# Optimization experiments

Hardware: AMD Instinct MI355X
Metric: run time of the kernel (lower is better)

The kernel has to match this reference:

```python
import jax, jax.numpy as jnp
import numpy as np

B, S, H, M, E = 64, 512, 1024, 26, 676  # batch, seq, hidden, max_nodes, max_edges (M*M)


def setup_inputs() -> dict:
    key = jax.random.key(0)
    ks = jax.random.split(key, 16)
    seq = jax.random.normal(ks[0], (B, S, H), jnp.float32)
    # ragged, strictly-increasing sentence-end offsets in [1, S-1], zero-padded tail
    rng = np.random.RandomState(0)
    off = np.zeros((B, M - 1), np.int64)
    for b in range(B):
        c = rng.randint(5, M)  # count of valid offsets per sample (ragged)
        off[b, :c] = np.sort(rng.choice(np.arange(1, S), size=c, replace=False))
    s = 1.0 / np.sqrt(H)
    s3 = 1.0 / np.sqrt(3 * H)
    return {
        'sequence_outputs': seq,
        'proof_offsets': jnp.asarray(off),
        'node_labels': jax.random.randint(ks[1], (B, M), 0, 2),
        'edge_labels': jax.random.randint(ks[2], (B, E), 0, 2),
        'W_naf': jax.random.normal(ks[3], (H, H), jnp.float32) * s,
        'b_naf': jnp.zeros((H,), jnp.float32),
        'W_cd': jax.random.normal(ks[4], (H, H), jnp.float32) * s,
        'b_cd': jnp.zeros((H,), jnp.float32),
        'W_co': jax.random.normal(ks[5], (H, 2), jnp.float32) * s,
        'b_co': jnp.zeros((2,), jnp.float32),
        'W_nd': jax.random.normal(ks[6], (H, H), jnp.float32) * s,
        'b_nd': jnp.zeros((H,), jnp.float32),
        'W_no': jax.random.normal(ks[7], (H, 2), jnp.float32) * s,
        'b_no': jnp.zeros((2,), jnp.float32),
        'W_ed': jax.random.normal(ks[8], (3 * H, H), jnp.float32) * s3,
        'b_ed': jnp.zeros((H,), jnp.float32),
        'W_eo': jax.random.normal(ks[9], (H, 2), jnp.float32) * s,
        'b_eo': jnp.zeros((2,), jnp.float32),
    }


def reference(sequence_outputs, proof_offsets, node_labels, edge_labels,
              W_naf, b_naf, W_cd, b_cd, W_co, b_co,
              W_nd, b_nd, W_no, b_no, W_ed, b_ed, W_eo, b_eo):
    Bx, Sx, Hx = sequence_outputs.shape
    Mx = node_labels.shape[1]
    Ex = edge_labels.shape[1]

    cls = sequence_outputs[:, 0, :]                       # [B,H]
    naf = cls @ W_naf + b_naf                             # NAF node embedding
    logits = jnp.tanh(cls @ W_cd + b_cd) @ W_co + b_co    # RobertaClassificationHead (eval: dropout=id)

    # segment-mean pooling via inclusive prefix sums: segment j = tokens (prev_j, off_j]
    P = jnp.cumsum(sequence_outputs, axis=1)              # [B,S,H]
    off = proof_offsets                                   # [B,M-1]
    prev = jnp.concatenate([jnp.zeros((Bx, 1), off.dtype), off[:, :-1]], axis=1)
    valid = off > 0                                       # [B,M-1]
    seg_sum = (jnp.take_along_axis(P, off[..., None], axis=1)
               - jnp.take_along_axis(P, prev[..., None], axis=1))  # [B,M-1,H]
    seg_len = jnp.maximum(off - prev, 1).astype(sequence_outputs.dtype)
    seg_mean = seg_sum / seg_len[..., None] * valid[..., None]

    count = valid.sum(axis=1)                             # nodes per sample (excl. NAF)
    # node embeddings: seg means at 0..count-1, NAF at index count, zeros after
    node_full = jnp.concatenate([seg_mean, jnp.zeros((Bx, 1, Hx), seg_mean.dtype)], axis=1)  # [B,M,H]
    idx = jnp.arange(Mx)
    node_full = node_full + (idx[None, :, None] == count[:, None, None]) * naf[:, None, :]

    # all-pairs edge features over n=count+1 nodes, row-major flat k=i*n+j, zero-padded to E
    n = count + 1                                         # [B]
    k = jnp.arange(Ex)                                    # [E]
    i = jnp.clip(k[None, :] // n[:, None], 0, Mx - 1)     # [B,E]
    j = jnp.clip(k[None, :] % n[:, None], 0, Mx - 1)
    valid_e = (k[None, :] < (n * n)[:, None])[..., None]
    ni = jnp.take_along_axis(node_full, i[..., None], axis=1)  # [B,E,H]
    nj = jnp.take_along_axis(node_full, j[..., None], axis=1)
    edge = jnp.concatenate([nj, ni, nj - ni], axis=-1) * valid_e  # [B,E,3H]

    node_logits = jnp.tanh(node_full @ W_nd + b_nd) @ W_no + b_no
    edge_logits = jnp.tanh(edge @ W_ed + b_ed) @ W_eo + b_eo
    return (logits, node_logits, edge_logits)
```

## Files before the change

kernel.cpp:

```cpp
#include <hip/hip_runtime.h>
#include <hip/hip_bf16.h>

#define B_ 64
#define S_ 512
#define H_ 1024
#define M_ 26
#define E_ 676

typedef short bf16x8 __attribute__((ext_vector_type(8)));
typedef float f32x4 __attribute__((ext_vector_type(4)));

__device__ __forceinline__ void gload16(const void* g, void* l) {
    __builtin_amdgcn_global_load_lds((const __attribute__((address_space(1))) unsigned int*)g,
                                     (__attribute__((address_space(3))) unsigned int*)l,
                                     16, 0, 0);
}

__device__ __forceinline__ float tanh_fast(float x) {
    float e = __expf(2.0f * x);
    return 1.0f - 2.0f * __builtin_amdgcn_rcpf(e + 1.0f);
}

__global__ __launch_bounds__(256) void k_stage1(
    const float* __restrict__ seq, const int* __restrict__ off,
    const float* __restrict__ Wnaf, const float* __restrict__ Wcd,
    const float* __restrict__ Wnd, const float* __restrict__ Wed,
    const float* __restrict__ bed, const float* __restrict__ Weo,
    const float* __restrict__ beo,
    __hip_bfloat16* __restrict__ Wt, int* __restrict__ count,
    float* __restrict__ econ, float* __restrict__ naf, float* __restrict__ cdh,
    float* __restrict__ node_sum) {
    __shared__ float smem[2048];
    int bid = blockIdx.x;
    int tid = threadIdx.x;

    if (bid < 2048) {
        int chunk = bid & 31, b = bid >> 5;
        int t0 = chunk * 16;
        const float4* sq = (const float4*)(seq + (size_t)b * S_ * H_);
        float4 buf[16];
#pragma unroll
        for (int i = 0; i < 16; ++i)
            buf[i] = sq[(size_t)(t0 + i) * (H_ / 4) + tid];

        int* offs = (int*)smem;
        int* cs = (int*)smem + 28;
        if (tid < M_ - 1) offs[tid] = off[b * (M_ - 1) + tid];
        __syncthreads();
        if (tid == 0) {
            int c = 0;
            while (c < M_ - 1 && offs[c] > 0) c++;
            cs[0] = c; cs[1] = (c > 0) ? offs[c - 1] : 0;
        }
        __syncthreads();
        int c = cs[0], offmax = cs[1];
        int ts = max(t0, 1), te = min(t0 + 15, offmax);
        int m = 0;
        while (m < c && offs[m] < ts) m++;
        float4 acc = make_float4(0, 0, 0, 0);
#pragma unroll
        for (int i = 0; i < 16; ++i) {
            int t = t0 + i;
            if (t < ts || t > te) continue;
            if (offs[m] < t) {
                float* dst = node_sum + ((size_t)(b * M_ + m)) * H_ + tid * 4;
                atomicAdd(dst + 0, acc.x); atomicAdd(dst + 1, acc.y);
                atomicAdd(dst + 2, acc.z); atomicAdd(dst + 3, acc.w);
                acc = make_float4(0, 0, 0, 0);
                while (offs[m] < t) m++;
            }
            acc.x += buf[i].x; acc.y += buf[i].y;
            acc.z += buf[i].z; acc.w += buf[i].w;
        }
        float* dst = node_sum + ((size_t)(b * M_ + m)) * H_ + tid * 4;
        atomicAdd(dst + 0, acc.x); atomicAdd(dst + 1, acc.y);
        atomicAdd(dst + 2, acc.z); atomicAdd(dst + 3, acc.w);
    } else if (bid < 2304) {
        float (*As)[64] = (float(*)[64])smem;
        float (*Bs)[64] = (float(*)[64])(smem + 1024);
        int e = bid - 2048;
        int bx = e & 31;
        int kbase = (e >> 5) * 128;
        const float* W;
        float* dst;
        int cbase;
        if (bx < 16) { W = Wnaf; dst = naf; cbase = bx * 64; }
        else         { W = Wcd;  dst = cdh; cbase = (bx - 16) * 64; }
        int tx = tid % 16, ty = tid / 16;
        float c[4][4] = {};
        int la_row = tid / 4;
        int la_k4  = (tid % 4) * 4;
        int lb_k   = tid / 16;
        int lb_c4  = (tid % 16) * 4;
        for (int k0 = 0; k0 < 128; k0 += 16) {
            float4 a = *(const float4*)(seq + (size_t)la_row * S_ * H_ + kbase + k0 + la_k4);
            *(float4*)(&Bs[lb_k][lb_c4]) =
                *(const float4*)(W + (size_t)(kbase + k0 + lb_k) * H_ + cbase + lb_c4);
            As[la_k4 + 0][la_row] = a.x;
            As[la_k4 + 1][la_row] = a.y;
            As[la_k4 + 2][la_row] = a.z;
            As[la_k4 + 3][la_row] = a.w;
            __syncthreads();
#pragma unroll
            for (int kk = 0; kk < 16; ++kk) {
                float4 av = *(const float4*)(&As[kk][ty * 4]);
                float4 bv = *(const float4*)(&Bs[kk][tx * 4]);
                c[0][0] += av.x * bv.x; c[0][1] += av.x * bv.y; c[0][2] += av.x * bv.z; c[0][3] += av.x * bv.w;
                c[1][0] += av.y * bv.x; c[1][1] += av.y * bv.y; c[1][2] += av.y * bv.z; c[1][3] += av.y * bv.w;
                c[2][0] += av.z * bv.x; c[2][1] += av.z * bv.y; c[2][2] += av.z * bv.z; c[2][3] += av.z * bv.w;
                c[3][0] += av.w * bv.x; c[3][1] += av.w * bv.y; c[3][2] += av.w * bv.z; c[3][3] += av.w * bv.w;
            }
            __syncthreads();
        }
#pragma unroll
        for (int i = 0; i < 4; ++i)
#pragma unroll
            for (int j = 0; j < 4; ++j)
                atomicAdd(dst + (size_t)(ty * 4 + i) * H_ + cbase + tx * 4 + j, c[i][j]);
    } else if (bid < 5376) {
        float (*T)[33] = (float(*)[33])smem;
        int idx = bid - 2304;
        int s = idx >> 10, rem = idx & 1023;
        int bx = rem & 31, by = rem >> 5;
        int c = tid & 31, r0 = tid >> 5;
        const int HH = H_ * H_;
#pragma unroll
        for (int i = 0; i < 4; ++i) {
            int r = r0 + 8 * i;
            size_t k = by * 32 + r, n = bx * 32 + c;
            float v;
            if (s == 0)      v = Wnd[k * H_ + n];
            else if (s == 1) v = Wed[k * H_ + n] + Wed[2 * HH + k * H_ + n];
            else             v = Wed[HH + k * H_ + n] - Wed[2 * HH + k * H_ + n];
            T[r][c] = v;
        }
        __syncthreads();
#pragma unroll
        for (int i = 0; i < 4; ++i) {
            int rr = r0 + 8 * i;
            Wt[(size_t)(s * H_ + bx * 32 + rr) * H_ + by * 32 + c] = __float2bfloat16(T[c][rr]);
        }
    } else if (bid == 5376) {
        if (tid < 64) {
            int b = tid;
            int c = 0;
            for (int m = 0; m < M_ - 1; ++m) c += (off[b * (M_ - 1) + m] > 0) ? 1 : 0;
            count[b] = c;
        }
    } else {
        float* s0 = smem; float* s1 = smem + 256;
        float a0 = 0.f, a1 = 0.f;
        for (int h = tid; h < H_; h += 256) {
            float t = tanh_fast(bed[h]);
            a0 += t * Weo[h * 2 + 0];
            a1 += t * Weo[h * 2 + 1];
        }
        s0[tid] = a0; s1[tid] = a1; __syncthreads();
        for (int o = 128; o > 0; o >>= 1) {
            if (tid < o) { s0[tid] += s0[tid + o]; s1[tid] += s1[tid + o]; }
            __syncthreads();
        }
        if (tid == 0) { econ[0] = s0[0] + beo[0]; econ[1] = s1[0] + beo[1]; }
    }
}

__global__ __launch_bounds__(256) void k_stage2(
    const float* __restrict__ sums, const int* __restrict__ off,
    const int* __restrict__ count, const float* __restrict__ naf,
    const float* __restrict__ bnaf, __hip_bfloat16* __restrict__ nodeB,
    const float* __restrict__ cdh, const float* __restrict__ bcd,
    const float* __restrict__ Wco, const float* __restrict__ bco,
    float* __restrict__ out) {
    __shared__ float smem[512];
    int bid = blockIdx.x;
    int tid = threadIdx.x;
    if (bid < 1664) {
        int b = bid / 26, m = bid - b * 26;
        int cnt = count[b];
        float4 v = make_float4(0, 0, 0, 0);
        const float4* row = (const float4*)(sums + ((size_t)(b * M_ + m)) * H_);
        if (m < M_ - 1) {
            int o = off[b * (M_ - 1) + m];
            if (o > 0) {
                int prev = (m > 0) ? off[b * (M_ - 1) + m - 1] : 0;
                float inv = 1.0f / (float)max(o - prev, 1);
                float4 s = row[tid];
                v = make_float4(s.x * inv, s.y * inv, s.z * inv, s.w * inv);
            }
        }
        if (m == cnt) {
            float4 a = ((const float4*)(naf + (size_t)b * H_))[tid];
            float4 bb = ((const float4*)bnaf)[tid];
            v.x += a.x + bb.x; v.y += a.y + bb.y; v.z += a.z + bb.z; v.w += a.w + bb.w;
        }
        __hip_bfloat16 __attribute__((aligned(8))) h[4] = {
            __float2bfloat16(v.x), __float2bfloat16(v.y),
            __float2bfloat16(v.z), __float2bfloat16(v.w)};
        *(ushort4*)(nodeB + ((size_t)(b * M_ + m)) * H_ + tid * 4) = *(const ushort4*)h;
    } else {
        int b = bid - 1664;
        float* s0 = smem; float* s1 = smem + 256;
        float a0 = 0.f, a1 = 0.f;
        for (int h = tid; h < H_; h += 256) {
            float t = tanh_fast(cdh[(size_t)b * H_ + h] + bcd[h]);
            a0 += t * Wco[h * 2 + 0];
            a1 += t * Wco[h * 2 + 1];
        }
        s0[tid] = a0; s1[tid] = a1; __syncthreads();
        for (int o = 128; o > 0; o >>= 1) {
            if (tid < o) { s0[tid] += s0[tid + o]; s1[tid] += s1[tid + o]; }
            __syncthreads();
        }
        if (tid == 0) { out[b * 2 + 0] = s0[0] + bco[0]; out[b * 2 + 1] = s1[0] + bco[1]; }
    }
}

#define GM 1664
#define GN 3072
#define GK 1024
__global__ __launch_bounds__(256) void k_mfma(const __hip_bfloat16* __restrict__ A,
                                              const __hip_bfloat16* __restrict__ Bt,
                                              float* __restrict__ C) {
    __shared__ __hip_bfloat16 As[128 * 32];
    __shared__ __hip_bfloat16 Bs[128 * 32];
    int tid = threadIdx.x;
    int wid = tid >> 6, ln = tid & 63;
    int row0 = blockIdx.y * 128, col0 = blockIdx.x * 128;
    const __hip_bfloat16* ga = A + (size_t)(row0 + wid * 16 + (ln >> 2)) * GK + (ln & 3) * 8;
    const __hip_bfloat16* gb = Bt + (size_t)(col0 + wid * 16 + (ln >> 2)) * GK + (ln & 3) * 8;
    __hip_bfloat16* lA = As + wid * 512;
    __hip_bfloat16* lB = Bs + wid * 512;
    int mrow = (wid >> 1) * 64, ncol = (wid & 1) * 64;
    int l15 = ln & 15, l4 = ln >> 4;
    f32x4 acc[4][4] = {};
    const __hip_bfloat16* pa = As + (size_t)(mrow + l15) * 32 + l4 * 8;
    const __hip_bfloat16* pb = Bs + (size_t)(ncol + l15) * 32 + l4 * 8;
    for (int k0 = 0; k0 < GK; k0 += 32) {
        gload16(ga, lA);
        gload16(ga + 64 * GK, lA + 2048);
        gload16(gb, lB);
        gload16(gb + 64 * GK, lB + 2048);
        ga += 32; gb += 32;
        __syncthreads();
        bf16x8 af[4], bf[4];
#pragma unroll
        for (int mi = 0; mi < 4; ++mi) af[mi] = *(const bf16x8*)(pa + mi * 16 * 32);
#pragma unroll
        for (int ni = 0; ni < 4; ++ni) bf[ni] = *(const bf16x8*)(pb + ni * 16 * 32);
#pragma unroll
        for (int mi = 0; mi < 4; ++mi)
#pragma unroll
            for (int ni = 0; ni < 4; ++ni)
                acc[mi][ni] = __builtin_amdgcn_mfma_f32_16x16x32_bf16(af[mi], bf[ni],
                                                                      acc[mi][ni], 0, 0, 0);
        __syncthreads();
    }
#pragma unroll
    for (int mi = 0; mi < 4; ++mi)
#pragma unroll
        for (int ni = 0; ni < 4; ++ni) {
            f32x4 v = acc[mi][ni];
            size_t r = row0 + mrow + mi * 16 + l4 * 4;
            size_t cc = col0 + ncol + ni * 16 + l15;
            C[(r + 0) * GN + cc] = v[0];
            C[(r + 1) * GN + cc] = v[1];
            C[(r + 2) * GN + cc] = v[2];
            C[(r + 3) * GN + cc] = v[3];
        }
}

__global__ __launch_bounds__(256) void k_stage4(
    const float* __restrict__ Cm, const int* __restrict__ count,
    const float* __restrict__ bnd, const float* __restrict__ Wno,
    const float* __restrict__ bno, const float* __restrict__ bed,
    const float* __restrict__ Weo, const float* __restrict__ beo,
    const float* __restrict__ econ, float* __restrict__ out_n,
    float* __restrict__ out_e) {
    int bid = blockIdx.x;
    int wid = threadIdx.x >> 6, lane = threadIdx.x & 63;
    if (bid < 416) {
        int r = bid * 4 + wid;
        const float4* src = (const float4*)(Cm + (size_t)r * GN);
        float a0 = 0.f, a1 = 0.f;
#pragma unroll
        for (int it = 0; it < 4; ++it) {
            int h = lane * 4 + it * 256;
            float4 s = src[lane + it * 64];
            float4 bb = *(const float4*)(bnd + h);
            float t0 = tanh_fast(s.x + bb.x), t1 = tanh_fast(s.y + bb.y);
            float t2 = tanh_fast(s.z + bb.z), t3 = tanh_fast(s.w + bb.w);
            a0 += t0 * Wno[h * 2 + 0] + t1 * Wno[h * 2 + 2] + t2 * Wno[h * 2 + 4] + t3 * Wno[h * 2 + 6];
            a1 += t0 * Wno[h * 2 + 1] + t1 * Wno[h * 2 + 3] + t2 * Wno[h * 2 + 5] + t3 * Wno[h * 2 + 7];
        }
        for (int o = 32; o > 0; o >>= 1) { a0 += __shfl_down(a0, o); a1 += __shfl_down(a1, o); }
        if (lane == 0) { out_n[(size_t)r * 2 + 0] = a0 + bno[0]; out_n[(size_t)r * 2 + 1] = a1 + bno[1]; }
    } else {
        int e = bid - 416;
        int b = e >> 4;
        int wg = (e & 15) * 4 + wid;
        int n = count[b] + 1;
        int n2 = n * n;
        float4 bed4[4], w04[4], w14[4];
#pragma unroll
        for (int it = 0; it < 4; ++it) {
            int h = lane * 4 + it * 256;
            bed4[it] = *(const float4*)(bed + h);
            w04[it] = make_float4(Weo[h * 2 + 0], Weo[h * 2 + 2], Weo[h * 2 + 4], Weo[h * 2 + 6]);
            w14[it] = make_float4(Weo[h * 2 + 1], Weo[h * 2 + 3], Weo[h * 2 + 5], Weo[h * 2 + 7]);
        }
        float e0 = econ[0], e1 = econ[1];
        float b0 = beo[0], b1 = beo[1];
        for (int k = wg; k < E_; k += 64) {
            float* dst = out_e + ((size_t)b * E_ + k) * 2;
            if (k >= n2) {
                if (lane == 0) { dst[0] = e0; dst[1] = e1; }
                continue;
            }
            int i = k / n, j = k - i * n;
            const float4* U4 = (const float4*)(Cm + (size_t)(b * M_ + j) * GN + H_);
            const float4* V4 = (const float4*)(Cm + (size_t)(b * M_ + i) * GN + 2 * H_);
            float a0 = 0.f, a1 = 0.f;
#pragma unroll
            for (int it = 0; it < 4; ++it) {
                float4 u = U4[lane + it * 64];
                float4 v = V4[lane + it * 64];
                float t0 = tanh_fast(u.x + v.x + bed4[it].x);
                float t1 = tanh_fast(u.y + v.y + bed4[it].y);
                float t2 = tanh_fast(u.z + v.z + bed4[it].z);
                float t3 = tanh_fast(u.w + v.w + bed4[it].w);
                a0 += t0 * w04[it].x + t1 * w04[it].y + t2 * w04[it].z + t3 * w04[it].w;
                a1 += t0 * w14[it].x + t1 * w14[it].y + t2 * w14[it].z + t3 * w14[it].w;
            }
            for (int o = 32; o > 0; o >>= 1) { a0 += __shfl_down(a0, o); a1 += __shfl_down(a1, o); }
            if (lane == 0) { dst[0] = a0 + b0; dst[1] = a1 + b1; }
        }
    }
}

extern "C" void kernel_launch(void* const* d_in, const int* in_sizes, int n_in,
                              void* d_out, int out_size, void* d_ws, size_t ws_size,
                              hipStream_t stream) {
    const float* seq  = (const float*)d_in[0];
    const int*   off  = (const int*)d_in[1];
    const float* Wnaf = (const float*)d_in[4];  const float* bnaf = (const float*)d_in[5];
    const float* Wcd  = (const float*)d_in[6];  const float* bcd  = (const float*)d_in[7];
    const float* Wco  = (const float*)d_in[8];  const float* bco  = (const float*)d_in[9];
    const float* Wnd  = (const float*)d_in[10]; const float* bnd  = (const float*)d_in[11];
    const float* Wno  = (const float*)d_in[12]; const float* bno  = (const float*)d_in[13];
    const float* Wed  = (const float*)d_in[14]; const float* bed  = (const float*)d_in[15];
    const float* Weo  = (const float*)d_in[16]; const float* beo  = (const float*)d_in[17];
    float* out = (float*)d_out;

    float* ws = (float*)d_ws;
    size_t p = 0;
    float* nodeS = ws + p;  p += (size_t)B_ * M_ * H_;
    float* naf   = ws + p;  p += (size_t)B_ * H_;
    float* cdh   = ws + p;  p += (size_t)B_ * H_;
    __hip_bfloat16* nodeB = (__hip_bfloat16*)(ws + p); p += (size_t)B_ * M_ * H_ / 2;
    __hip_bfloat16* Wt    = (__hip_bfloat16*)(ws + p); p += (size_t)3 * H_ * H_ / 2;
    float* Cbuf  = ws + p;  p += (size_t)B_ * M_ * 3 * H_;
    int*   cnt   = (int*)(ws + p); p += 64;
    float* econ  = ws + p;  p += 2;

    hipMemsetAsync(nodeS, 0, ((size_t)B_ * M_ * H_ + 2 * (size_t)B_ * H_) * sizeof(float),
                   stream);

    k_stage1<<<dim3(5378), 256, 0, stream>>>(seq, off, Wnaf, Wcd, Wnd, Wed, bed, Weo, beo,
                                             Wt, cnt, econ, naf, cdh, nodeS);
    k_stage2<<<dim3(1728), 256, 0, stream>>>(nodeS, off, cnt, naf, bnaf, nodeB,
                                             cdh, bcd, Wco, bco, out);
    k_mfma<<<dim3(GN / 128, GM / 128), 256, 0, stream>>>(nodeB, Wt, Cbuf);
    k_stage4<<<dim3(1440), 256, 0, stream>>>(Cbuf, cnt, bnd, Wno, bno, bed, Weo, beo, econ,
                                             out + B_ * 2, out + B_ * 2 + B_ * M_ * 2);
}
```

Before: 314.7 us.

## Split segment pooling into own kernel with async global-to-LDS loads

Segment-sum pooling moves out of the fused stage-1 kernel into a dedicated kernel. It uses 8-token chunks (4096 blocks) loaded directly into LDS via global_load_lds, and returns early for chunks beyond the last offset. The remaining stage-1 work (small GEMMs, weight transpose, counts) runs as a separate launch. This aims to cut register pressure from the 16-float4 buffer, raise occupancy, and skip padded tokens, at the cost of an extra kernel launch and a serialization point between the two kernels.

```diff
diff --git a/kernel.cpp b/kernel.cpp
--- a/kernel.cpp
+++ b/kernel.cpp
@@ -21,64 +21,73 @@
     return 1.0f - 2.0f * __builtin_amdgcn_rcpf(e + 1.0f);
 }
 
-__global__ __launch_bounds__(256) void k_stage1(
+__global__ __launch_bounds__(256) void k_seg(
+    const float* __restrict__ seq, const int* __restrict__ off,
+    float* __restrict__ node_sum) {
+    __shared__ float rows[8 * 1024];
+    __shared__ int offs[26];
+    __shared__ int cs[2];
+    int bid = blockIdx.x;
+    int tid = threadIdx.x;
+    int chunk = bid & 63, b = bid >> 6;
+    int t0 = chunk * 8;
+    int wid = tid >> 6;
+
+    const float* sq = seq + (size_t)b * S_ * H_ + (size_t)t0 * H_ + tid * 4;
+    float* ld = rows + wid * 256;
+#pragma unroll
+    for (int i = 0; i < 8; ++i)
+        gload16(sq + i * H_, ld + i * 1024);
+
+    if (tid < M_ - 1) offs[tid] = off[b * (M_ - 1) + tid];
+    __syncthreads();
+    if (tid == 0) {
+        int c = 0;
+        while (c < M_ - 1 && offs[c] > 0) c++;
+        cs[0] = c; cs[1] = (c > 0) ? offs[c - 1] : 0;
+    }
+    __syncthreads();
+    int c = cs[0], offmax = cs[1];
+    int ts = max(t0, 1), te = min(t0 + 7, offmax);
+    if (ts > te) return;
+    int m = 0;
+    while (m < c && offs[m] < ts) m++;
+    float4 acc = make_float4(0, 0, 0, 0);
+#pragma unroll
+    for (int i = 0; i < 8; ++i) {
+        int t = t0 + i;
+        if (t < ts || t > te) continue;
+        if (offs[m] < t) {
+            float* dst = node_sum + ((size_t)(b * M_ + m)) * H_ + tid * 4;
+            atomicAdd(dst + 0, acc.x); atomicAdd(dst + 1, acc.y);
+            atomicAdd(dst + 2, acc.z); atomicAdd(dst + 3, acc.w);
+            acc = make_float4(0, 0, 0, 0);
+            while (offs[m] < t) m++;
+        }
+        float4 v = *(const float4*)(rows + i * 1024 + tid * 4);
+        acc.x += v.x; acc.y += v.y; acc.z += v.z; acc.w += v.w;
+    }
+    float* dst = node_sum + ((size_t)(b * M_ + m)) * H_ + tid * 4;
+    atomicAdd(dst + 0, acc.x); atomicAdd(dst + 1, acc.y);
+    atomicAdd(dst + 2, acc.z); atomicAdd(dst + 3, acc.w);
+}
+
+__global__ __launch_bounds__(256) void k_stage1b(
     const float* __restrict__ seq, const int* __restrict__ off,
     const float* __restrict__ Wnaf, const float* __restrict__ Wcd,
     const float* __restrict__ Wnd, const float* __restrict__ Wed,
     const float* __restrict__ bed, const float* __restrict__ Weo,
     const float* __restrict__ beo,
     __hip_bfloat16* __restrict__ Wt, int* __restrict__ count,
-    float* __restrict__ econ, float* __restrict__ naf, float* __restrict__ cdh,
-    float* __restrict__ node_sum) {
+    float* __restrict__ econ, float* __restrict__ naf, float* __restrict__ cdh) {
     __shared__ float smem[2048];
     int bid = blockIdx.x;
     int tid = threadIdx.x;
 
-    if (bid < 2048) {
-        int chunk = bid & 31, b = bid >> 5;
-        int t0 = chunk * 16;
-        const float4* sq = (const float4*)(seq + (size_t)b * S_ * H_);
-        float4 buf[16];
-#pragma unroll
-        for (int i = 0; i < 16; ++i)
-            buf[i] = sq[(size_t)(t0 + i) * (H_ / 4) + tid];
-
-        int* offs = (int*)smem;
-        int* cs = (int*)smem + 28;
-        if (tid < M_ - 1) offs[tid] = off[b * (M_ - 1) + tid];
-        __syncthreads();
-        if (tid == 0) {
-            int c = 0;
-            while (c < M_ - 1 && offs[c] > 0) c++;
-            cs[0] = c; cs[1] = (c > 0) ? offs[c - 1] : 0;
-        }
-        __syncthreads();
-        int c = cs[0], offmax = cs[1];
-        int ts = max(t0, 1), te = min(t0 + 15, offmax);
-        int m = 0;
-        while (m < c && offs[m] < ts) m++;
-        float4 acc = make_float4(0, 0, 0, 0);
-#pragma unroll
-        for (int i = 0; i < 16; ++i) {
-            int t = t0 + i;
-            if (t < ts || t > te) continue;
-            if (offs[m] < t) {
-                float* dst = node_sum + ((size_t)(b * M_ + m)) * H_ + tid * 4;
-                atomicAdd(dst + 0, acc.x); atomicAdd(dst + 1, acc.y);
-                atomicAdd(dst + 2, acc.z); atomicAdd(dst + 3, acc.w);
-                acc = make_float4(0, 0, 0, 0);
-                while (offs[m] < t) m++;
-            }
-            acc.x += buf[i].x; acc.y += buf[i].y;
-            acc.z += buf[i].z; acc.w += buf[i].w;
-        }
-        float* dst = node_sum + ((size_t)(b * M_ + m)) * H_ + tid * 4;
-        atomicAdd(dst + 0, acc.x); atomicAdd(dst + 1, acc.y);
-        atomicAdd(dst + 2, acc.z); atomicAdd(dst + 3, acc.w);
-    } else if (bid < 2304) {
+    if (bid < 256) {
         float (*As)[64] = (float(*)[64])smem;
         float (*Bs)[64] = (float(*)[64])(smem + 1024);
-        int e = bid - 2048;
+        int e = bid;
         int bx = e & 31;
         int kbase = (e >> 5) * 128;
         const float* W;
@@ -117,9 +126,9 @@
 #pragma unroll
             for (int j = 0; j < 4; ++j)
                 atomicAdd(dst + (size_t)(ty * 4 + i) * H_ + cbase + tx * 4 + j, c[i][j]);
-    } else if (bid < 5376) {
+    } else if (bid < 3328) {
         float (*T)[33] = (float(*)[33])smem;
-        int idx = bid - 2304;
+        int idx = bid - 256;
         int s = idx >> 10, rem = idx & 1023;
         int bx = rem & 31, by = rem >> 5;
         int c = tid & 31, r0 = tid >> 5;
@@ -140,7 +149,7 @@
             int rr = r0 + 8 * i;
             Wt[(size_t)(s * H_ + bx * 32 + rr) * H_ + by * 32 + c] = __float2bfloat16(T[c][rr]);
         }
-    } else if (bid == 5376) {
+    } else if (bid == 3328) {
         if (tid < 64) {
             int b = tid;
             int c = 0;
@@ -365,8 +374,9 @@
     hipMemsetAsync(nodeS, 0, ((size_t)B_ * M_ * H_ + 2 * (size_t)B_ * H_) * sizeof(float),
                    stream);
 
-    k_stage1<<<dim3(5378), 256, 0, stream>>>(seq, off, Wnaf, Wcd, Wnd, Wed, bed, Weo, beo,
-                                             Wt, cnt, econ, naf, cdh, nodeS);
+    k_seg<<<dim3(4096), 256, 0, stream>>>(seq, off, nodeS);
+    k_stage1b<<<dim3(3330), 256, 0, stream>>>(seq, off, Wnaf, Wcd, Wnd, Wed, bed, Weo, beo,
+                                              Wt, cnt, econ, naf, cdh);
     k_stage2<<<dim3(1728), 256, 0, stream>>>(nodeS, off, cnt, naf, bnaf, nodeB,
                                              cdh, bcd, Wco, bco, out);
     k_mfma<<<dim3(GN / 128, GM / 128), 256, 0, stream>>>(nodeB, Wt, Cbuf);
```

Result: slower. 349.0 us (+10.9%).
